# Kernel optimization log

Hardware: AMD Instinct MI355X
Metric: run time of the kernel (lower is better)

Reference implementation:

```python
import jax, jax.numpy as jnp
import numpy as np

T, B, IN_DIM, H, N_RESETS = 4096, 256, 128, 8, 32


def setup_inputs() -> dict:
    key = jax.random.key(0)
    ks = jax.random.split(key, 8)
    s = 1.0 / np.sqrt(H)  # PyTorch LSTM/Linear init scale
    return {
        "x": jax.random.normal(ks[0], (T, B, IN_DIM), jnp.float32),
        "reset_idx": jnp.sort(jax.random.randint(ks[1], (N_RESETS,), 0, T)),
        "W_ih": jax.random.uniform(ks[2], (4 * H, IN_DIM), jnp.float32, -s, s),
        "W_hh": jax.random.uniform(ks[3], (4 * H, H), jnp.float32, -s, s),
        "b_ih": jax.random.uniform(ks[4], (4 * H,), jnp.float32, -s, s),
        "b_hh": jax.random.uniform(ks[5], (4 * H,), jnp.float32, -s, s),
        "W_proj": jax.random.uniform(ks[6], (1, H), jnp.float32, -s, s),
        "b_proj": jax.random.uniform(ks[7], (1,), jnp.float32, -s, s),
    }


def reference(x, reset_idx, W_ih, W_hh, b_ih, b_hh, W_proj, b_proj):
    # x: [T, B, in_dim] (batch_first=False).  reset_idx: timesteps where the
    # LSTM hidden/cell state is reset to zero before processing that step.
    Tn = x.shape[0]
    Bn = x.shape[1]
    Hn = W_hh.shape[1]
    reset_mask = jnp.zeros((Tn,), dtype=bool).at[reset_idx].set(True)

    # Precompute the input contribution to the gates for all timesteps at once
    # (this is the bulk of the FLOPs; only the small HxH recurrence stays in scan).
    x_gates = jnp.einsum("tbi,gi->tbg", x, W_ih) + b_ih + b_hh  # [T, B, 4H]

    def step(carry, inp):
        h, c = carry  # [B, H] each
        xg, rt = inp  # [B, 4H], scalar bool
        h = jnp.where(rt, jnp.zeros_like(h), h)
        c = jnp.where(rt, jnp.zeros_like(c), c)
        gates = xg + h @ W_hh.T  # [B, 4H]
        i, f, g, o = jnp.split(gates, 4, axis=-1)  # PyTorch gate order i,f,g,o
        c = jax.nn.sigmoid(f) * c + jax.nn.sigmoid(i) * jnp.tanh(g)
        h = jax.nn.sigmoid(o) * jnp.tanh(c)
        return (h, c), h

    h0 = jnp.zeros((Bn, Hn), x.dtype)
    c0 = jnp.zeros((Bn, Hn), x.dtype)
    (_, _), rnn_out = jax.lax.scan(step, (h0, c0), (x_gates, reset_mask))

    value = rnn_out @ W_proj.T + b_proj  # [T, B, 1]
    return (value, rnn_out)
```

## Files before the change

kernel.cpp:

```cpp
#include <hip/hip_runtime.h>
#include <cstdint>

#define TT 4096
#define BB 256
#define ID 128

typedef float f32x4 __attribute__((ext_vector_type(4)));
typedef short s16x8 __attribute__((ext_vector_type(8)));
typedef _Float16 h16x4 __attribute__((ext_vector_type(4)));

__device__ __forceinline__ float rcp_fast(float x) { return __builtin_amdgcn_rcpf(x); }
__device__ __forceinline__ float sigm(float x) { return rcp_fast(1.0f + __expf(-x)); }
__device__ __forceinline__ float tanh_fast(float x) {
  float e = __expf(2.0f * x);
  return 1.0f - 2.0f * rcp_fast(e + 1.0f);
}

union U16B { uint32_t u[4]; s16x8 v; };

__device__ __forceinline__ void split8(const float4 a, const float4 b,
                                       s16x8& hi, s16x8& lo) {
  uint32_t a0 = __float_as_uint(a.x), a1 = __float_as_uint(a.y);
  uint32_t a2 = __float_as_uint(a.z), a3 = __float_as_uint(a.w);
  uint32_t b0 = __float_as_uint(b.x), b1 = __float_as_uint(b.y);
  uint32_t b2 = __float_as_uint(b.z), b3 = __float_as_uint(b.w);
  U16B h;
  h.u[0] = (a0 >> 16) | (a1 & 0xffff0000u);
  h.u[1] = (a2 >> 16) | (a3 & 0xffff0000u);
  h.u[2] = (b0 >> 16) | (b1 & 0xffff0000u);
  h.u[3] = (b2 >> 16) | (b3 & 0xffff0000u);
  hi = h.v;
  float r0 = a.x - __uint_as_float(a0 & 0xffff0000u);
  float r1 = a.y - __uint_as_float(a1 & 0xffff0000u);
  float r2 = a.z - __uint_as_float(a2 & 0xffff0000u);
  float r3 = a.w - __uint_as_float(a3 & 0xffff0000u);
  float r4 = b.x - __uint_as_float(b0 & 0xffff0000u);
  float r5 = b.y - __uint_as_float(b1 & 0xffff0000u);
  float r6 = b.z - __uint_as_float(b2 & 0xffff0000u);
  float r7 = b.w - __uint_as_float(b3 & 0xffff0000u);
  U16B l;
  l.u[0] = (__float_as_uint(r0) >> 16) | (__float_as_uint(r1) & 0xffff0000u);
  l.u[1] = (__float_as_uint(r2) >> 16) | (__float_as_uint(r3) & 0xffff0000u);
  l.u[2] = (__float_as_uint(r4) >> 16) | (__float_as_uint(r5) & 0xffff0000u);
  l.u[3] = (__float_as_uint(r6) >> 16) | (__float_as_uint(r7) & 0xffff0000u);
  lo = l.v;
}

__global__ __launch_bounds__(64) void prep_kernel(
    const float* __restrict__ W_ih, const float* __restrict__ b_ih,
    const float* __restrict__ b_hh,
    s16x8* __restrict__ whi, s16x8* __restrict__ wlo, float4* __restrict__ bo4)
{
  const int lane = threadIdx.x;
  const int c    = lane & 15;
  const int kq   = (lane >> 4) * 2;
  const float4* __restrict__ w4 = reinterpret_cast<const float4*>(W_ih);
#pragma unroll
  for (int kc = 0; kc < 4; ++kc) {
#pragma unroll
    for (int nf = 0; nf < 2; ++nf) {
      int gA = (c & 3) * 8 + nf * 4 + (c >> 2);
      int q0 = kc * 8 + kq;
      float4 wa = w4[gA * 32 + q0];
      float4 wb = w4[gA * 32 + q0 + 1];
      s16x8 hi, lo;
      split8(wa, wb, hi, lo);
      whi[(kc * 2 + nf) * 64 + lane] = hi;
      wlo[(kc * 2 + nf) * 64 + lane] = lo;
    }
  }
  if (lane < 8) {
    float4 b;
    b.x = b_ih[lane]      + b_hh[lane];
    b.y = b_ih[8 + lane]  + b_hh[8 + lane];
    b.z = b_ih[16 + lane] + b_hh[16 + lane];
    b.w = b_ih[24 + lane] + b_hh[24 + lane];
    bo4[lane] = b;
  }
}

__global__ __launch_bounds__(256) void gates_kernel(
    const float* __restrict__ x,
    const s16x8* __restrict__ whi, const s16x8* __restrict__ wlo,
    const float4* __restrict__ bo4, _Float16* __restrict__ xg)
{
  __shared__ float4 xt[64 * 32];
  const int tid = threadIdx.x;
  const size_t row0 = (size_t)blockIdx.x * 64;

  const float4* __restrict__ src = reinterpret_cast<const float4*>(x) + row0 * 32;
#pragma unroll
  for (int it = 0; it < 8; ++it) {
    int idx = it * 256 + tid;
    int r = idx >> 5, q = idx & 31;
    xt[r * 32 + (q ^ (r & 31))] = src[idx];
  }

  const int lane = tid & 63;
  const int wv   = tid >> 6;
  const int rloc = wv * 16 + (lane & 15);
  const int kq   = (lane >> 4) * 2;

  s16x8 Wh[4][2], Wl[4][2];
#pragma unroll
  for (int kc = 0; kc < 4; ++kc) {
#pragma unroll
    for (int nf = 0; nf < 2; ++nf) {
      Wh[kc][nf] = whi[(kc * 2 + nf) * 64 + lane];
      Wl[kc][nf] = wlo[(kc * 2 + nf) * 64 + lane];
    }
  }
  const int qD = lane >> 4;
  const float4 bq0 = bo4[qD];
  const float4 bq1 = bo4[4 + qD];

  __syncthreads();

  f32x4 acc[2] = {{0.f, 0.f, 0.f, 0.f}, {0.f, 0.f, 0.f, 0.f}};
#pragma unroll
  for (int kc = 0; kc < 4; ++kc) {
    int q0 = kc * 8 + kq;
    float4 xa = xt[rloc * 32 + (q0 ^ (rloc & 31))];
    float4 xb = xt[rloc * 32 + ((q0 + 1) ^ (rloc & 31))];
    s16x8 Xh, Xl;
    split8(xa, xb, Xh, Xl);
#pragma unroll
    for (int nf = 0; nf < 2; ++nf) {
      acc[nf] = __builtin_amdgcn_mfma_f32_16x16x32_bf16(Wh[kc][nf], Xh, acc[nf], 0, 0, 0);
      acc[nf] = __builtin_amdgcn_mfma_f32_16x16x32_bf16(Wl[kc][nf], Xh, acc[nf], 0, 0, 0);
      acc[nf] = __builtin_amdgcn_mfma_f32_16x16x32_bf16(Wh[kc][nf], Xl, acc[nf], 0, 0, 0);
    }
  }

  const int c_ = lane & 15;
  h16x4* __restrict__ xgh = reinterpret_cast<h16x4*>(xg);
  const size_t xrow = row0 + wv * 16 + c_;
  {
    h16x4 hv;
    hv[0] = (_Float16)(acc[0][0] + bq0.x);
    hv[1] = (_Float16)(acc[0][1] + bq0.y);
    hv[2] = (_Float16)(acc[0][2] + bq0.z);
    hv[3] = (_Float16)(acc[0][3] + bq0.w);
    xgh[xrow * 8 + qD] = hv;
  }
  {
    h16x4 hv;
    hv[0] = (_Float16)(acc[1][0] + bq1.x);
    hv[1] = (_Float16)(acc[1][1] + bq1.y);
    hv[2] = (_Float16)(acc[1][2] + bq1.z);
    hv[3] = (_Float16)(acc[1][3] + bq1.w);
    xgh[xrow * 8 + 4 + qD] = hv;
  }
}

__global__ __launch_bounds__(64) void rnn_kernel(
    const _Float16* __restrict__ xg, const int* __restrict__ reset_idx,
    const float* __restrict__ W_hh, const float* __restrict__ W_proj,
    const float* __restrict__ b_proj, float* __restrict__ out)
{
  const int seg  = blockIdx.x;
  const int lane = threadIdx.x;
  const int j    = lane & 7;
  const int b    = blockIdx.y * 8 + (lane >> 3);

  const int start = (seg == 0)  ? 0  : reset_idx[seg - 1];
  const int end   = (seg == 32) ? TT : reset_idx[seg];
  if (start >= end) return;

  float wi[8], wf[8], wg_[8], wo[8];
#pragma unroll
  for (int k = 0; k < 8; ++k) {
    wi[k]  = W_hh[(0  + j) * 8 + k];
    wf[k]  = W_hh[(8  + j) * 8 + k];
    wg_[k] = W_hh[(16 + j) * 8 + k];
    wo[k]  = W_hh[(24 + j) * 8 + k];
  }
  const float bp = b_proj[0];
  float wp[8];
#pragma unroll
  for (int k = 0; k < 8; ++k) wp[k] = W_proj[k];

  float h[8];
#pragma unroll
  for (int k = 0; k < 8; ++k) h[k] = 0.f;
  float c = 0.f;

  float* __restrict__ vout = out;
  float* __restrict__ hout = out + (size_t)TT * BB;

  const h16x4* __restrict__ xgh4 = reinterpret_cast<const h16x4*>(xg);
  const size_t lbase = (size_t)b * 8 + j;

  h16x4 bufA[8], bufB[8];

#define LOADC(buf, tc) do {                                                  \
  _Pragma("unroll")                                                          \
  for (int s = 0; s < 8; ++s) {                                              \
    int tt = (tc) + s; tt = tt < TT ? tt : TT - 1;   \
    (buf)[s] = xgh4[(size_t)tt * 2048 + lbase];                              \
  }                                                                          \
} while (0)

#define STEP8(buf, tc) do {                                                  \
  _Pragma("unroll")                                                          \
  for (int s = 0; s < 8; ++s) {                                              \
    int t = (tc) + s;                                                        \
    if (t < end) {                                  \
      float gi = (float)(buf)[s][0], gf = (float)(buf)[s][1];                \
      float gg = (float)(buf)[s][2], go = (float)(buf)[s][3];                \
      float gi1 = 0.f, gf1 = 0.f, gg1 = 0.f, go1 = 0.f;                      \
      _Pragma("unroll")                                                      \
      for (int k = 0; k < 8; k += 2) {                                       \
        gi += wi[k]  * h[k];  gi1 += wi[k+1]  * h[k+1];                      \
        gf += wf[k]  * h[k];  gf1 += wf[k+1]  * h[k+1];                      \
        gg += wg_[k] * h[k];  gg1 += wg_[k+1] * h[k+1];                      \
        go += wo[k]  * h[k];  go1 += wo[k+1]  * h[k+1];                      \
      }                                                                      \
      gi += gi1; gf += gf1; gg += gg1; go += go1;                            \
      float si = sigm(gi), sf = sigm(gf), sg = tanh_fast(gg), so = sigm(go); \
      c = sf * c + si * sg;                                                  \
      float hj = so * tanh_fast(c);                                          \
      hout[((size_t)t * BB + b) * 8 + j] = hj;                               \
      _Pragma("unroll")                                                      \
      for (int k = 0; k < 8; ++k) h[k] = __shfl(hj, k, 8);                   \
      float sv = bp;                                                         \
      _Pragma("unroll")                                                      \
      for (int k = 0; k < 8; ++k) sv += wp[k] * h[k];                        \
      if (j == 0) vout[(size_t)t * BB + b] = sv;                             \
    }                                                                        \
  }                                                                          \
} while (0)

  LOADC(bufA, start);
  LOADC(bufB, start + 8);
  for (int tc = start; tc < end; tc += 16) {
    STEP8(bufA, tc);
    LOADC(bufA, tc + 16);
    STEP8(bufB, tc + 8);
    LOADC(bufB, tc + 24);
  }
#undef LOADC
#undef STEP8
}

extern "C" void kernel_launch(void* const* d_in, const int* in_sizes, int n_in,
                              void* d_out, int out_size, void* d_ws, size_t ws_size,
                              hipStream_t stream) {
  const float* x      = (const float*)d_in[0];
  const int*   ridx   = (const int*)  d_in[1];
  const float* W_ih   = (const float*)d_in[2];
  const float* W_hh   = (const float*)d_in[3];
  const float* b_ih   = (const float*)d_in[4];
  const float* b_hh   = (const float*)d_in[5];
  const float* W_proj = (const float*)d_in[6];
  const float* b_proj = (const float*)d_in[7];
  float* out = (float*)d_out;

  _Float16* xg  = (_Float16*)d_ws;
  char*  aux = (char*)d_ws + (size_t)134217728;
  s16x8* whi = (s16x8*)aux;
  s16x8* wlo = whi + 512;
  float4* bo4 = (float4*)(wlo + 512);

  prep_kernel<<<1, 64, 0, stream>>>(W_ih, b_ih, b_hh, whi, wlo, bo4);
  gates_kernel<<<(TT * BB) / 64, 256, 0, stream>>>(x, whi, wlo, bo4, xg);
  rnn_kernel<<<dim3(33, 32), 64, 0, stream>>>(xg, ridx, W_hh, W_proj, b_proj, out);
}
```

Before: 256.9 us.

## Fuse input-gate GEMM into recurrent scan kernel via LDS double buffering

```diff
diff --git a/kernel.cpp b/kernel.cpp
--- a/kernel.cpp
+++ b/kernel.cpp
@@ -3,11 +3,9 @@
 
 #define TT 4096
 #define BB 256
-#define ID 128
 
 typedef float f32x4 __attribute__((ext_vector_type(4)));
 typedef short s16x8 __attribute__((ext_vector_type(8)));
-typedef _Float16 h16x4 __attribute__((ext_vector_type(4)));
 
 __device__ __forceinline__ float rcp_fast(float x) { return __builtin_amdgcn_rcpf(x); }
 __device__ __forceinline__ float sigm(float x) { return rcp_fast(1.0f + __expf(-x)); }
@@ -79,93 +77,39 @@
   }
 }
 
-__global__ __launch_bounds__(256) void gates_kernel(
-    const float* __restrict__ x,
+__global__ __launch_bounds__(64) void fused_kernel(
+    const float* __restrict__ x, const int* __restrict__ reset_idx,
     const s16x8* __restrict__ whi, const s16x8* __restrict__ wlo,
-    const float4* __restrict__ bo4, _Float16* __restrict__ xg)
-{
-  __shared__ float4 xt[64 * 32];
-  const int tid = threadIdx.x;
-  const size_t row0 = (size_t)blockIdx.x * 64;
-
-  const float4* __restrict__ src = reinterpret_cast<const float4*>(x) + row0 * 32;
-#pragma unroll
-  for (int it = 0; it < 8; ++it) {
-    int idx = it * 256 + tid;
-    int r = idx >> 5, q = idx & 31;
-    xt[r * 32 + (q ^ (r & 31))] = src[idx];
-  }
-
-  const int lane = tid & 63;
-  const int wv   = tid >> 6;
-  const int rloc = wv * 16 + (lane & 15);
-  const int kq   = (lane >> 4) * 2;
-
-  s16x8 Wh[4][2], Wl[4][2];
-#pragma unroll
-  for (int kc = 0; kc < 4; ++kc) {
-#pragma unroll
-    for (int nf = 0; nf < 2; ++nf) {
-      Wh[kc][nf] = whi[(kc * 2 + nf) * 64 + lane];
-      Wl[kc][nf] = wlo[(kc * 2 + nf) * 64 + lane];
-    }
-  }
-  const int qD = lane >> 4;
-  const float4 bq0 = bo4[qD];
-  const float4 bq1 = bo4[4 + qD];
-
-  __syncthreads();
-
-  f32x4 acc[2] = {{0.f, 0.f, 0.f, 0.f}, {0.f, 0.f, 0.f, 0.f}};
-#pragma unroll
-  for (int kc = 0; kc < 4; ++kc) {
-    int q0 = kc * 8 + kq;
-    float4 xa = xt[rloc * 32 + (q0 ^ (rloc & 31))];
-    float4 xb = xt[rloc * 32 + ((q0 + 1) ^ (rloc & 31))];
-    s16x8 Xh, Xl;
-    split8(xa, xb, Xh, Xl);
-#pragma unroll
-    for (int nf = 0; nf < 2; ++nf) {
-      acc[nf] = __builtin_amdgcn_mfma_f32_16x16x32_bf16(Wh[kc][nf], Xh, acc[nf], 0, 0, 0);
-      acc[nf] = __builtin_amdgcn_mfma_f32_16x16x32_bf16(Wl[kc][nf], Xh, acc[nf], 0, 0, 0);
-      acc[nf] = __builtin_amdgcn_mfma_f32_16x16x32_bf16(Wh[kc][nf], Xl, acc[nf], 0, 0, 0);
-    }
-  }
-
-  const int c_ = lane & 15;
-  h16x4* __restrict__ xgh = reinterpret_cast<h16x4*>(xg);
-  const size_t xrow = row0 + wv * 16 + c_;
-  {
-    h16x4 hv;
-    hv[0] = (_Float16)(acc[0][0] + bq0.x);
-    hv[1] = (_Float16)(acc[0][1] + bq0.y);
-    hv[2] = (_Float16)(acc[0][2] + bq0.z);
-    hv[3] = (_Float16)(acc[0][3] + bq0.w);
-    xgh[xrow * 8 + qD] = hv;
-  }
-  {
-    h16x4 hv;
-    hv[0] = (_Float16)(acc[1][0] + bq1.x);
-    hv[1] = (_Float16)(acc[1][1] + bq1.y);
-    hv[2] = (_Float16)(acc[1][2] + bq1.z);
-    hv[3] = (_Float16)(acc[1][3] + bq1.w);
-    xgh[xrow * 8 + 4 + qD] = hv;
-  }
-}
-
-__global__ __launch_bounds__(64) void rnn_kernel(
-    const _Float16* __restrict__ xg, const int* __restrict__ reset_idx,
+    const float4* __restrict__ bo4,
     const float* __restrict__ W_hh, const float* __restrict__ W_proj,
     const float* __restrict__ b_proj, float* __restrict__ out)
 {
   const int seg  = blockIdx.x;
   const int lane = threadIdx.x;
-  const int j    = lane & 7;
-  const int b    = blockIdx.y * 8 + (lane >> 3);
+  const int b0   = blockIdx.y * 8;
 
   const int start = (seg == 0)  ? 0  : reset_idx[seg - 1];
   const int end   = (seg == 32) ? TT : reset_idx[seg];
   if (start >= end) return;
+
+  const int cD = lane & 15;
+  const int qD = lane >> 4;
+  s16x8 Wh[4][2], Wl[4][2];
+#pragma unroll
+  for (int kc = 0; kc < 4; ++kc) {
+#pragma unroll
+    for (int nf = 0; nf < 2; ++nf) {
+      Wh[kc][nf] = whi[(kc * 2 + nf) * 64 + lane];
+      Wl[kc][nf] = wlo[(kc * 2 + nf) * 64 + lane];
+    }
+  }
+  const float4 bq0 = bo4[qD];
+  const float4 bq1 = bo4[4 + qD];
+  const float4* __restrict__ x4 = reinterpret_cast<const float4*>(x);
+
+  const int j    = lane & 7;
+  const int bsub = lane >> 3;
+  const int b    = b0 + bsub;
 
   float wi[8], wf[8], wg_[8], wo[8];
 #pragma unroll
@@ -188,59 +132,87 @@
   float* __restrict__ vout = out;
   float* __restrict__ hout = out + (size_t)TT * BB;
 
-  const h16x4* __restrict__ xgh4 = reinterpret_cast<const h16x4*>(xg);
-  const size_t lbase = (size_t)b * 8 + j;
-
-  h16x4 bufA[8], bufB[8];
-
-#define LOADC(buf, tc) do {                                                  \
-  _Pragma("unroll")                                                          \
-  for (int s = 0; s < 8; ++s) {                                              \
-    int tt = (tc) + s; tt = tt < TT ? tt : TT - 1;   \
-    (buf)[s] = xgh4[(size_t)tt * 2048 + lbase];                              \
-  }                                                                          \
-} while (0)
-
-#define STEP8(buf, tc) do {                                                  \
-  _Pragma("unroll")                                                          \
-  for (int s = 0; s < 8; ++s) {                                              \
-    int t = (tc) + s;                                                        \
-    if (t < end) {                                  \
-      float gi = (float)(buf)[s][0], gf = (float)(buf)[s][1];                \
-      float gg = (float)(buf)[s][2], go = (float)(buf)[s][3];                \
-      float gi1 = 0.f, gf1 = 0.f, gg1 = 0.f, go1 = 0.f;                      \
-      _Pragma("unroll")                                                      \
-      for (int k = 0; k < 8; k += 2) {                                       \
-        gi += wi[k]  * h[k];  gi1 += wi[k+1]  * h[k+1];                      \
-        gf += wf[k]  * h[k];  gf1 += wf[k+1]  * h[k+1];                      \
-        gg += wg_[k] * h[k];  gg1 += wg_[k+1] * h[k+1];                      \
-        go += wo[k]  * h[k];  go1 += wo[k+1]  * h[k+1];                      \
-      }                                                                      \
-      gi += gi1; gf += gf1; gg += gg1; go += go1;                            \
-      float si = sigm(gi), sf = sigm(gf), sg = tanh_fast(gg), so = sigm(go); \
-      c = sf * c + si * sg;                                                  \
-      float hj = so * tanh_fast(c);                                          \
-      hout[((size_t)t * BB + b) * 8 + j] = hj;                               \
-      _Pragma("unroll")                                                      \
-      for (int k = 0; k < 8; ++k) h[k] = __shfl(hj, k, 8);                   \
-      float sv = bp;                                                         \
-      _Pragma("unroll")                                                      \
-      for (int k = 0; k < 8; ++k) sv += wp[k] * h[k];                        \
-      if (j == 0) vout[(size_t)t * BB + b] = sv;                             \
-    }                                                                        \
-  }                                                                          \
-} while (0)
-
-  LOADC(bufA, start);
-  LOADC(bufB, start + 8);
+  __shared__ float4 glA[8 * 8 * 8];
+  __shared__ float4 glB[8 * 8 * 8];
+
+#define GEMM8(gl, tc0) do {                                                    \
+    _Pragma("unroll")                                                          \
+    for (int tile_ = 0; tile_ < 4; ++tile_) {                                  \
+      int t_ = (tc0) + tile_ * 2 + (cD >> 3);                                  \
+      t_ = t_ < TT ? t_ : TT - 1;                     \
+      const size_t rb_ = ((size_t)t_ * BB + b0 + (cD & 7)) * 32;               \
+      f32x4 a0_ = {0.f, 0.f, 0.f, 0.f}, a1_ = {0.f, 0.f, 0.f, 0.f};           \
+      _Pragma("unroll")                                                        \
+      for (int kc_ = 0; kc_ < 4; ++kc_) {                                      \
+        float4 xa_ = x4[rb_ + kc_ * 8 + qD * 2];                               \
+        float4 xb_ = x4[rb_ + kc_ * 8 + qD * 2 + 1];                           \
+        s16x8 Xh_, Xl_;                                                        \
+        split8(xa_, xb_, Xh_, Xl_);                                            \
+        a0_ = __builtin_amdgcn_mfma_f32_16x16x32_bf16(Wh[kc_][0], Xh_, a0_, 0, 0, 0); \
+        a0_ = __builtin_amdgcn_mfma_f32_16x16x32_bf16(Wl[kc_][0], Xh_, a0_, 0, 0, 0); \
+        a0_ = __builtin_amdgcn_mfma_f32_16x16x32_bf16(Wh[kc_][0], Xl_, a0_, 0, 0, 0); \
+        a1_ = __builtin_amdgcn_mfma_f32_16x16x32_bf16(Wh[kc_][1], Xh_, a1_, 0, 0, 0); \
+        a1_ = __builtin_amdgcn_mfma_f32_16x16x32_bf16(Wl[kc_][1], Xh_, a1_, 0, 0, 0); \
+        a1_ = __builtin_amdgcn_mfma_f32_16x16x32_bf16(Wh[kc_][1], Xl_, a1_, 0, 0, 0); \
+      }                                                                        \
+      const int tl_ = tile_ * 2 + (cD >> 3);                                   \
+      const int bl_ = cD & 7;                                                  \
+      const int rr_ = (tl_ * 8 + bl_) * 8;                                     \
+      float4 v0_;                                                              \
+      v0_.x = a0_[0] + bq0.x; v0_.y = a0_[1] + bq0.y;                          \
+      v0_.z = a0_[2] + bq0.z; v0_.w = a0_[3] + bq0.w;                          \
+      (gl)[rr_ + (qD ^ bl_)] = v0_;                                            \
+      float4 v1_;                                                              \
+      v1_.x = a1_[0] + bq1.x; v1_.y = a1_[1] + bq1.y;                          \
+      v1_.z = a1_[2] + bq1.z; v1_.w = a1_[3] + bq1.w;                          \
+      (gl)[rr_ + ((4 + qD) ^ bl_)] = v1_;                                      \
+    }                                                                          \
+  } while (0)
+
+#define SCAN8(gl, tc0) do {                                                    \
+    float4 g_[8];                                                              \
+    _Pragma("unroll")                                                          \
+    for (int s_ = 0; s_ < 8; ++s_)                                             \
+      g_[s_] = (gl)[(s_ * 8 + bsub) * 8 + (j ^ bsub)];                         \
+    _Pragma("unroll")                                                          \
+    for (int s_ = 0; s_ < 8; ++s_) {                                           \
+      int t_ = (tc0) + s_;                                                     \
+      if (t_ < end) {                                 \
+        float gi = g_[s_].x, gf = g_[s_].y;                                    \
+        float gg = g_[s_].z, go = g_[s_].w;                                    \
+        float gi1 = 0.f, gf1 = 0.f, gg1 = 0.f, go1 = 0.f;                      \
+        _Pragma("unroll")                                                      \
+        for (int k = 0; k < 8; k += 2) {                                       \
+          gi += wi[k]  * h[k];  gi1 += wi[k+1]  * h[k+1];                      \
+          gf += wf[k]  * h[k];  gf1 += wf[k+1]  * h[k+1];                      \
+          gg += wg_[k] * h[k];  gg1 += wg_[k+1] * h[k+1];                      \
+          go += wo[k]  * h[k];  go1 += wo[k+1]  * h[k+1];                      \
+        }                                                                      \
+        gi += gi1; gf += gf1; gg += gg1; go += go1;                            \
+        float si = sigm(gi), sf = sigm(gf), sg = tanh_fast(gg), so = sigm(go); \
+        c = sf * c + si * sg;                                                  \
+        float hj = so * tanh_fast(c);                                          \
+        hout[((size_t)t_ * BB + b) * 8 + j] = hj;                              \
+        _Pragma("unroll")                                                      \
+        for (int k = 0; k < 8; ++k) h[k] = __shfl(hj, k, 8);                   \
+        float sv = bp;                                                         \
+        _Pragma("unroll")                                                      \
+        for (int k = 0; k < 8; ++k) sv += wp[k] * h[k];                        \
+        if (j == 0) vout[(size_t)t_ * BB + b] = sv;                            \
+      }                                                                        \
+    }                                                                          \
+  } while (0)
+
+  GEMM8(glA, start);
+  GEMM8(glB, start + 8);
   for (int tc = start; tc < end; tc += 16) {
-    STEP8(bufA, tc);
-    LOADC(bufA, tc + 16);
-    STEP8(bufB, tc + 8);
-    LOADC(bufB, tc + 24);
-  }
-#undef LOADC
-#undef STEP8
+    SCAN8(glA, tc);
+    if (tc + 16 < end) GEMM8(glA, tc + 16);
+    SCAN8(glB, tc + 8);
+    if (tc + 24 < end) GEMM8(glB, tc + 24);
+  }
+#undef GEMM8
+#undef SCAN8
 }
 
 extern "C" void kernel_launch(void* const* d_in, const int* in_sizes, int n_in,
@@ -256,13 +228,11 @@
   const float* b_proj = (const float*)d_in[7];
   float* out = (float*)d_out;
 
-  _Float16* xg  = (_Float16*)d_ws;
-  char*  aux = (char*)d_ws + (size_t)134217728;
-  s16x8* whi = (s16x8*)aux;
+  s16x8* whi = (s16x8*)d_ws;
   s16x8* wlo = whi + 512;
   float4* bo4 = (float4*)(wlo + 512);
 
   prep_kernel<<<1, 64, 0, stream>>>(W_ih, b_ih, b_hh, whi, wlo, bo4);
-  gates_kernel<<<(TT * BB) / 64, 256, 0, stream>>>(x, whi, wlo, bo4, xg);
-  rnn_kernel<<<dim3(33, 32), 64, 0, stream>>>(xg, ridx, W_hh, W_proj, b_proj, out);
-}
+  fused_kernel<<<dim3(33, 32), 64, 0, stream>>>(x, ridx, whi, wlo, bo4,
+                                                W_hh, W_proj, b_proj, out);
+}
```

Result: slower. 453.9 us (+76.7%).
